# Kernel optimization log

Hardware: AMD Instinct MI355X
Metric: run time of the kernel (lower is better)

The kernel has to match this reference:

```python
import math
import jax, jax.numpy as jnp
import numpy as np

B, S, D, H = 4, 1024, 512, 8
DH = D // H  # 64
SQRT_DIM = math.sqrt(D)


def _relative_shift(pos_score):
    # pos_score: [B, H, S, S]
    b, h, s1, s2 = pos_score.shape
    zeros = jnp.zeros((b, h, s1, 1), dtype=pos_score.dtype)
    padded = jnp.concatenate([zeros, pos_score], axis=-1)      # [B,H,S,S+1]
    padded = padded.reshape(b, h, s2 + 1, s1)                  # [B,H,S+1,S]
    return padded[:, :, 1:].reshape(b, h, s1, s2)


def setup_inputs() -> dict:
    key = jax.random.key(0)
    ks = jax.random.split(key, 14)
    std = 0.02
    inp = {
        "query": jax.random.normal(ks[0], (B, S, D), jnp.float32),
        "key": jax.random.normal(ks[1], (B, S, D), jnp.float32),
        "value": jax.random.normal(ks[2], (B, S, D), jnp.float32),
        "pos_embedding": jax.random.normal(ks[3], (B, S, D), jnp.float32),
        # projection weights stored [in, out] so y = x @ W + b
        "Wq": jax.random.normal(ks[4], (D, D), jnp.float32) * std,
        "bq": jnp.zeros((D,), jnp.float32),
        "Wk": jax.random.normal(ks[5], (D, D), jnp.float32) * std,
        "bk": jnp.zeros((D,), jnp.float32),
        "Wv": jax.random.normal(ks[6], (D, D), jnp.float32) * std,
        "bv": jnp.zeros((D,), jnp.float32),
        "Wp": jax.random.normal(ks[7], (D, D), jnp.float32) * std,  # pos_proj, no bias
        "Wo": jax.random.normal(ks[8], (D, D), jnp.float32) * std,
        "bo": jnp.zeros((D,), jnp.float32),
        "u_bias": jax.random.normal(ks[9], (H, DH), jnp.float32) * std,
        "v_bias": jax.random.normal(ks[10], (H, DH), jnp.float32) * std,
    }
    return inp


def reference(query, key, value, pos_embedding, Wq, bq, Wk, bk, Wv, bv, Wp, Wo, bo, u_bias, v_bias):
    b = query.shape[0]
    q = (query @ Wq + bq).reshape(b, -1, H, DH)          # [B,S,H,DH]
    k = (key @ Wk + bk).reshape(b, -1, H, DH)            # [B,T,H,DH]
    v = (value @ Wv + bv).reshape(b, -1, H, DH)          # [B,T,H,DH]
    p = (pos_embedding @ Wp).reshape(b, -1, H, DH)       # [B,T,H,DH]

    # content score: (q + u) . k  -> [B,H,S,T]
    content_score = jnp.einsum('bshd,bthd->bhst', q + u_bias, k)
    # position score: (q + v) . pos -> [B,H,S,T], then relative shift
    pos_score = jnp.einsum('bshd,bthd->bhst', q + v_bias, p)
    pos_score = _relative_shift(pos_score)

    score = (content_score + pos_score) / SQRT_DIM
    attn = jax.nn.softmax(score, axis=-1)                # dropout p=0 (eval)

    context = jnp.einsum('bhst,bthd->bshd', attn, v).reshape(b, -1, D)
    out = context @ Wo + bo
    return (out, attn)
```

## Files before the change

kernel.cpp:

```cpp
#include <hip/hip_runtime.h>

#define B_  4
#define S_  1024
#define D_  512
#define H_  8
#define DH_ 64
#define SCALE 0.044194173824159216f

typedef short bf16x8 __attribute__((ext_vector_type(8)));
typedef float f32x4  __attribute__((ext_vector_type(4)));

__device__ __forceinline__ unsigned short f2bf(float x) {
    union { float f; unsigned int u; } v; v.f = x;
    unsigned int r = v.u + 0x7fffu + ((v.u >> 16) & 1u);
    return (unsigned short)(r >> 16);
}
__device__ __forceinline__ float bf2f(unsigned short h) {
    union { unsigned int u; float f; } v; v.u = ((unsigned int)h) << 16;
    return v.f;
}

__global__ __launch_bounds__(256) void convert_wt_k(
    const float* __restrict__ W0, const float* __restrict__ W1,
    const float* __restrict__ W2, const float* __restrict__ W3,
    const float* __restrict__ W4,
    unsigned short* __restrict__ T0, unsigned short* __restrict__ T1,
    unsigned short* __restrict__ T2, unsigned short* __restrict__ T3,
    unsigned short* __restrict__ T4)
{
    const float* W;
    unsigned short* T;
    switch (blockIdx.y) {
        case 0: W = W0; T = T0; break;
        case 1: W = W1; T = T1; break;
        case 2: W = W2; T = T2; break;
        case 3: W = W3; T = T3; break;
        default: W = W4; T = T4; break;
    }
    const int e = blockIdx.x * 256 + threadIdx.x;
    const int o = e >> 9, i = e & 511;
    T[(size_t)o * 512 + i] = f2bf(W[(size_t)i * 512 + o]);
}

__global__ __launch_bounds__(256) void proj_all_k(
    const float* __restrict__ Aq_, const float* __restrict__ Ak_,
    const float* __restrict__ Ap_, const float* __restrict__ Av_,
    const unsigned short* __restrict__ WqT, const unsigned short* __restrict__ WkT,
    const unsigned short* __restrict__ WpT, const unsigned short* __restrict__ WvT,
    const float* __restrict__ bq, const float* __restrict__ bk,
    const float* __restrict__ bv,
    const float* __restrict__ ub, const float* __restrict__ vb,
    unsigned short* __restrict__ qu, unsigned short* __restrict__ qv,
    unsigned short* __restrict__ kbf, unsigned short* __restrict__ pbf,
    unsigned short* __restrict__ vT)
{
    __shared__ unsigned short Ab[64][72];
    __shared__ unsigned short Bb[64][72];
    const int mode = blockIdx.z;
    const float* A;
    const unsigned short* BT;
    switch (mode) {
        case 0: A = Aq_; BT = WqT; break;
        case 1: A = Ak_; BT = WkT; break;
        case 2: A = Ap_; BT = WpT; break;
        default: A = Av_; BT = WvT; break;
    }
    const int tid = threadIdx.x;
    const int i0 = blockIdx.x * 64, j0 = blockIdx.y * 64;
    const int w = tid >> 6, lane = tid & 63, l15 = lane & 15, lhi = lane >> 4;
    const int mr0 = (w >> 1) * 32, nc0 = (w & 1) * 32;
    f32x4 acc[2][2] = {};

    for (int k0 = 0; k0 < 512; k0 += 64) {
        __syncthreads();
#pragma unroll
        for (int it = 0; it < 4; ++it) {
            const int s = tid + it * 256;
            const int row = s >> 4, f4 = (s & 15) * 4;
            float4 va = *(const float4*)&A[(size_t)(i0 + row) * 512 + k0 + f4];
            ushort4 hh;
            hh.x = f2bf(va.x); hh.y = f2bf(va.y); hh.z = f2bf(va.z); hh.w = f2bf(va.w);
            *(ushort4*)&Ab[row][f4] = hh;
        }
#pragma unroll
        for (int it = 0; it < 2; ++it) {
            const int s = tid + it * 256;
            const int row = s >> 3, g = (s & 7) * 8;
            *(bf16x8*)&Bb[row][g] = *(const bf16x8*)&BT[(size_t)(j0 + row) * 512 + k0 + g];
        }
        __syncthreads();
#pragma unroll
        for (int kk = 0; kk < 2; ++kk) {
            bf16x8 a0 = *(const bf16x8*)&Ab[mr0 + l15][kk * 32 + lhi * 8];
            bf16x8 a1 = *(const bf16x8*)&Ab[mr0 + 16 + l15][kk * 32 + lhi * 8];
            bf16x8 b0 = *(const bf16x8*)&Bb[nc0 + l15][kk * 32 + lhi * 8];
            bf16x8 b1 = *(const bf16x8*)&Bb[nc0 + 16 + l15][kk * 32 + lhi * 8];
            acc[0][0] = __builtin_amdgcn_mfma_f32_16x16x32_bf16(a0, b0, acc[0][0], 0, 0, 0);
            acc[0][1] = __builtin_amdgcn_mfma_f32_16x16x32_bf16(a0, b1, acc[0][1], 0, 0, 0);
            acc[1][0] = __builtin_amdgcn_mfma_f32_16x16x32_bf16(a1, b0, acc[1][0], 0, 0, 0);
            acc[1][1] = __builtin_amdgcn_mfma_f32_16x16x32_bf16(a1, b1, acc[1][1], 0, 0, 0);
        }
    }

#pragma unroll
    for (int m = 0; m < 2; ++m)
#pragma unroll
        for (int n = 0; n < 2; ++n)
#pragma unroll
            for (int r = 0; r < 4; ++r) {
                const int grow = i0 + mr0 + 16 * m + 4 * lhi + r;
                const int gcol = j0 + nc0 + 16 * n + l15;
                const int b = grow >> 10, s = grow & 1023;
                const int h = gcol >> 6, d = gcol & 63;
                const float v = acc[m][n][r];
                if (mode == 3) {
                    const size_t idx = (((size_t)(b * H_ + h)) * DH_ + d) * S_ + s;
                    vT[idx] = f2bf(v + bv[gcol]);
                } else {
                    const size_t idx = (((size_t)b * H_ + h) * S_ + s) * DH_ + d;
                    if (mode == 0) {
                        const float base = v + bq[gcol];
                        qu[idx] = f2bf(base + ub[gcol]);
                        qv[idx] = f2bf(base + vb[gcol]);
                    } else if (mode == 1) {
                        kbf[idx] = f2bf(v + bk[gcol]);
                    } else {
                        pbf[idx] = f2bf(v);
                    }
                }
            }
}

__global__ __launch_bounds__(256) void gemm_bf16_k(
    const unsigned short* __restrict__ A,
    const unsigned short* __restrict__ BT,
    const float* __restrict__ bias,
    float* __restrict__ C)
{
    __shared__ unsigned short Ab[64][72];
    __shared__ unsigned short Bb[64][72];
    const int tid = threadIdx.x;
    const int i0 = blockIdx.x * 64, j0 = blockIdx.y * 64;
    const int w = tid >> 6, lane = tid & 63, l15 = lane & 15, lhi = lane >> 4;
    const int mr0 = (w >> 1) * 32, nc0 = (w & 1) * 32;
    f32x4 acc[2][2] = {};

    for (int k0 = 0; k0 < 512; k0 += 64) {
        __syncthreads();
#pragma unroll
        for (int it = 0; it < 2; ++it) {
            const int s = tid + it * 256;
            const int row = s >> 3, g = (s & 7) * 8;
            *(bf16x8*)&Ab[row][g] = *(const bf16x8*)&A[(size_t)(i0 + row) * 512 + k0 + g];
            *(bf16x8*)&Bb[row][g] = *(const bf16x8*)&BT[(size_t)(j0 + row) * 512 + k0 + g];
        }
        __syncthreads();
#pragma unroll
        for (int kk = 0; kk < 2; ++kk) {
            bf16x8 a0 = *(const bf16x8*)&Ab[mr0 + l15][kk * 32 + lhi * 8];
            bf16x8 a1 = *(const bf16x8*)&Ab[mr0 + 16 + l15][kk * 32 + lhi * 8];
            bf16x8 b0 = *(const bf16x8*)&Bb[nc0 + l15][kk * 32 + lhi * 8];
            bf16x8 b1 = *(const bf16x8*)&Bb[nc0 + 16 + l15][kk * 32 + lhi * 8];
            acc[0][0] = __builtin_amdgcn_mfma_f32_16x16x32_bf16(a0, b0, acc[0][0], 0, 0, 0);
            acc[0][1] = __builtin_amdgcn_mfma_f32_16x16x32_bf16(a0, b1, acc[0][1], 0, 0, 0);
            acc[1][0] = __builtin_amdgcn_mfma_f32_16x16x32_bf16(a1, b0, acc[1][0], 0, 0, 0);
            acc[1][1] = __builtin_amdgcn_mfma_f32_16x16x32_bf16(a1, b1, acc[1][1], 0, 0, 0);
        }
    }

#pragma unroll
    for (int m = 0; m < 2; ++m)
#pragma unroll
        for (int n = 0; n < 2; ++n)
#pragma unroll
            for (int r = 0; r < 4; ++r) {
                const int grow = i0 + mr0 + 16 * m + 4 * lhi + r;
                const int gcol = j0 + nc0 + 16 * n + l15;
                C[(size_t)grow * 512 + gcol] = acc[m][n][r] + bias[gcol];
            }
}

#define RS 1032
#define QBLK 16

__global__ __launch_bounds__(512, 4) void score_fused_k(
    const unsigned short* __restrict__ qu_g,
    const unsigned short* __restrict__ qv_g,
    const unsigned short* __restrict__ kb_g,
    const unsigned short* __restrict__ pb_g,
    const unsigned short* __restrict__ vT_g,
    float* __restrict__ attn,
    unsigned short* __restrict__ ctx_g)
{
    __shared__ unsigned short Qu[16][72];
    __shared__ unsigned short Aq[32][72];
    __shared__ unsigned short Kb[128][72];
    __shared__ unsigned short Pb[128][72];
    __shared__ unsigned short Rfl[17 * RS];
    __shared__ float red[16][9];

    const int tid = threadIdx.x;
    const int i0 = blockIdx.x * QBLK;
    const int bh = blockIdx.y;
    const int w = tid >> 6, lane = tid & 63, l15 = lane & 15, lhi = lane >> 4;

    const unsigned short* qu_b = qu_g + (size_t)bh * S_ * DH_;
    const unsigned short* qv_b = qv_g + (size_t)bh * S_ * DH_;
    const unsigned short* kb_b = kb_g + (size_t)bh * S_ * DH_;
    const unsigned short* pb_b = pb_g + (size_t)bh * S_ * DH_;

    if (tid < 128) {
        const int r = tid >> 3, seg = (tid & 7) * 8;
        *(bf16x8*)&Qu[r][seg] = *(const bf16x8*)&qu_b[(size_t)(i0 + r) * DH_ + seg];
    }
    if (tid < 256) {
        const int r = tid >> 3, seg = (tid & 7) * 8;
        const int src = min(i0 + r, S_ - 1);
        *(bf16x8*)&Aq[r][seg] = *(const bf16x8*)&qv_b[(size_t)src * DH_ + seg];
    }

    bf16x8 kreg[2], preg[2];
#pragma unroll
    for (int it = 0; it < 2; ++it) {
        const int s = tid + it * 512;
        const int row = s >> 3, seg = (s & 7) * 8;
        kreg[it] = *(const bf16x8*)&kb_b[(size_t)row * DH_ + seg];
        preg[it] = *(const bf16x8*)&pb_b[(size_t)row * DH_ + seg];
    }

    f32x4 acc[8] = {};
    for (int jc = 0; jc < 8; ++jc) {
        __syncthreads();
#pragma unroll
        for (int it = 0; it < 2; ++it) {
            const int s = tid + it * 512;
            const int row = s >> 3, seg = (s & 7) * 8;
            *(bf16x8*)&Kb[row][seg] = kreg[it];
            *(bf16x8*)&Pb[row][seg] = preg[it];
        }
        if (jc < 7) {
#pragma unroll
            for (int it = 0; it < 2; ++it) {
                const int s = tid + it * 512;
                const int row = (jc + 1) * 128 + (s >> 3), seg = (s & 7) * 8;
                kreg[it] = *(const bf16x8*)&kb_b[(size_t)row * DH_ + seg];
                preg[it] = *(const bf16x8*)&pb_b[(size_t)row * DH_ + seg];
            }
        }
        __syncthreads();

        f32x4 racc[2] = {};
#pragma unroll
        for (int kk = 0; kk < 2; ++kk) {
            bf16x8 pfr = *(const bf16x8*)&Pb[16 * w + l15][kk * 32 + lhi * 8];
            bf16x8 kfr = *(const bf16x8*)&Kb[16 * w + l15][kk * 32 + lhi * 8];
            bf16x8 aq0 = *(const bf16x8*)&Aq[l15][kk * 32 + lhi * 8];
            bf16x8 aq1 = *(const bf16x8*)&Aq[16 + l15][kk * 32 + lhi * 8];
            bf16x8 qf  = *(const bf16x8*)&Qu[l15][kk * 32 + lhi * 8];
            racc[0] = __builtin_amdgcn_mfma_f32_16x16x32_bf16(aq0, pfr, racc[0], 0, 0, 0);
            racc[1] = __builtin_amdgcn_mfma_f32_16x16x32_bf16(aq1, pfr, racc[1], 0, 0, 0);
            acc[jc] = __builtin_amdgcn_mfma_f32_16x16x32_bf16(qf,  kfr, acc[jc], 0, 0, 0);
        }
#pragma unroll
        for (int m = 0; m < 2; ++m)
#pragma unroll
            for (int r = 0; r < 4; ++r) {
                const int row = 16 * m + 4 * lhi + r;
                if (row < 17)
                    Rfl[row * RS + jc * 128 + 16 * w + l15] = f2bf(racc[m][r]);
            }
    }
    __syncthreads();

    const int il = 4 * lhi;
    float rmax[4], rsum[4];
#pragma unroll
    for (int r = 0; r < 4; ++r) rmax[r] = -3.0e38f;

#pragma unroll
    for (int jc = 0; jc < 8; ++jc)
#pragma unroll
        for (int r = 0; r < 4; ++r) {
            const int row = il + r;
            const int i = i0 + row;
            const int j = jc * 128 + 16 * w + l15;
            float pos = 0.f;
            if (j <= i)          pos = bf2f(Rfl[row * RS + 1023 - i + j]);
            else if (j >= i + 2) pos = bf2f(Rfl[(row + 1) * RS + (j - i - 2)]);
            const float s = (acc[jc][r] + pos) * SCALE;
            acc[jc][r] = s;
            rmax[r] = fmaxf(rmax[r], s);
        }

#pragma unroll
    for (int r = 0; r < 4; ++r)
#pragma unroll
        for (int off = 1; off < 16; off <<= 1)
            rmax[r] = fmaxf(rmax[r], __shfl_xor(rmax[r], off));
    if (l15 == 0)
#pragma unroll
        for (int r = 0; r < 4; ++r) red[il + r][w] = rmax[r];
    __syncthreads();
#pragma unroll
    for (int r = 0; r < 4; ++r) {
        float mx = red[il + r][0];
#pragma unroll
        for (int ww = 1; ww < 8; ++ww) mx = fmaxf(mx, red[il + r][ww]);
        rmax[r] = mx;
        rsum[r] = 0.f;
    }
    __syncthreads();

#pragma unroll
    for (int jc = 0; jc < 8; ++jc)
#pragma unroll
        for (int r = 0; r < 4; ++r) {
            const float e = __expf(acc[jc][r] - rmax[r]);
            acc[jc][r] = e;
            rsum[r] += e;
        }
#pragma unroll
    for (int r = 0; r < 4; ++r)
#pragma unroll
        for (int off = 1; off < 16; off <<= 1)
            rsum[r] += __shfl_xor(rsum[r], off);
    if (l15 == 0)
#pragma unroll
        for (int r = 0; r < 4; ++r) red[il + r][w] = rsum[r];
    __syncthreads();

    float* attn_b = attn + (size_t)bh * S_ * S_;
#pragma unroll
    for (int r = 0; r < 4; ++r) {
        float sum = red[il + r][0];
#pragma unroll
        for (int ww = 1; ww < 8; ++ww) sum += red[il + r][ww];
        const float inv = 1.f / sum;
#pragma unroll
        for (int jc = 0; jc < 8; ++jc) {
            const int j = jc * 128 + 16 * w + l15;
            const float pn = acc[jc][r] * inv;
            attn_b[(size_t)(i0 + il + r) * S_ + j] = pn;
            Rfl[(il + r) * RS + j] = f2bf(pn);
        }
    }
    __syncthreads();

    const int b4 = bh >> 3, h4 = bh & 7;
    const int nblk = w & 3;
    const int kh = w >> 2;
    const unsigned short* vrow = vT_g + (size_t)bh * DH_ * S_
                               + (size_t)(16 * nblk + l15) * S_;
    f32x4 cacc = {};
#pragma unroll
    for (int ki = 0; ki < 16; ++ki) {
        const int t0 = kh * 512 + ki * 32 + lhi * 8;
        bf16x8 a  = *(const bf16x8*)&Rfl[l15 * RS + t0];
        bf16x8 bb = *(const bf16x8*)&vrow[t0];
        cacc = __builtin_amdgcn_mfma_f32_16x16x32_bf16(a, bb, cacc, 0, 0, 0);
    }
    float* fred = (float*)&Kb[0][0];
    if (kh == 0) {
#pragma unroll
        for (int r = 0; r < 4; ++r)
            fred[(nblk * 16 + 4 * lhi + r) * 16 + l15] = cacc[r];
    }
    __syncthreads();
    if (kh == 1) {
#pragma unroll
        for (int r = 0; r < 4; ++r) {
            const float vs = cacc[r] + fred[(nblk * 16 + 4 * lhi + r) * 16 + l15];
            const int srow = i0 + 4 * lhi + r;
            ctx_g[((size_t)(b4 * S_ + srow)) * D_ + h4 * DH_ + 16 * nblk + l15] = f2bf(vs);
        }
    }
}

extern "C" void kernel_launch(void* const* d_in, const int* in_sizes, int n_in,
                              void* d_out, int out_size, void* d_ws, size_t ws_size,
                              hipStream_t stream)
{
    const float* query = (const float*)d_in[0];
    const float* key_  = (const float*)d_in[1];
    const float* value = (const float*)d_in[2];
    const float* pose  = (const float*)d_in[3];
    const float* Wq = (const float*)d_in[4];
    const float* bq = (const float*)d_in[5];
    const float* Wk = (const float*)d_in[6];
    const float* bk = (const float*)d_in[7];
    const float* Wv = (const float*)d_in[8];
    const float* bv = (const float*)d_in[9];
    const float* Wp = (const float*)d_in[10];
    const float* Wo = (const float*)d_in[11];
    const float* bo = (const float*)d_in[12];
    const float* u_bias = (const float*)d_in[13];
    const float* v_bias = (const float*)d_in[14];

    const size_t NTOK = (size_t)B_ * S_ * D_;
    float* out  = (float*)d_out;
    float* attn = (float*)d_out + NTOK;

    unsigned short* qu  = (unsigned short*)d_ws;
    unsigned short* qv  = qu + NTOK;
    unsigned short* kbf = qv + NTOK;
    unsigned short* pbf = kbf + NTOK;
    unsigned short* WqT = pbf + NTOK;
    unsigned short* WkT = WqT + 262144;
    unsigned short* WpT = WkT + 262144;
    unsigned short* WvT = WpT + 262144;
    unsigned short* WoT = WvT + 262144;
    unsigned short* vT  = WoT + 262144;
    unsigned short* ctx = vT + NTOK;

    const dim3 blk256(256);
    const dim3 gproj(64, 8);

    convert_wt_k<<<dim3(1024, 5), blk256, 0, stream>>>(Wq, Wk, Wp, Wv, Wo,
                                                       WqT, WkT, WpT, WvT, WoT);

    proj_all_k<<<dim3(64, 8, 4), blk256, 0, stream>>>(
        query, key_, pose, value,
        WqT, WkT, WpT, WvT,
        bq, bk, bv, u_bias, v_bias,
        qu, qv, kbf, pbf, vT);

    score_fused_k<<<dim3(S_ / QBLK, B_ * H_), dim3(512), 0, stream>>>(
        qu, qv, kbf, pbf, vT, attn, ctx);

    gemm_bf16_k<<<gproj, blk256, 0, stream>>>(ctx, WoT, bo, out);
}
```

Before: 138.0 us.

## Tile weight transpose, block V layout, scatter shifted pos scores directly

```diff
diff --git a/kernel.cpp b/kernel.cpp
--- a/kernel.cpp
+++ b/kernel.cpp
@@ -28,18 +28,25 @@
     unsigned short* __restrict__ T2, unsigned short* __restrict__ T3,
     unsigned short* __restrict__ T4)
 {
+    __shared__ float tile[64][65];
     const float* W;
     unsigned short* T;
-    switch (blockIdx.y) {
+    switch (blockIdx.z) {
         case 0: W = W0; T = T0; break;
         case 1: W = W1; T = T1; break;
         case 2: W = W2; T = T2; break;
         case 3: W = W3; T = T3; break;
         default: W = W4; T = T4; break;
     }
-    const int e = blockIdx.x * 256 + threadIdx.x;
-    const int o = e >> 9, i = e & 511;
-    T[(size_t)o * 512 + i] = f2bf(W[(size_t)i * 512 + o]);
+    const int r0 = blockIdx.y * 64, c0 = blockIdx.x * 64;
+    const int tx = threadIdx.x & 63, ty = threadIdx.x >> 6;
+#pragma unroll
+    for (int it = 0; it < 16; ++it)
+        tile[ty + 4 * it][tx] = W[(size_t)(r0 + ty + 4 * it) * 512 + c0 + tx];
+    __syncthreads();
+#pragma unroll
+    for (int it = 0; it < 16; ++it)
+        T[(size_t)(c0 + ty + 4 * it) * 512 + r0 + tx] = f2bf(tile[tx][ty + 4 * it]);
 }
 
 __global__ __launch_bounds__(256) void proj_all_k(
@@ -52,7 +59,7 @@
     const float* __restrict__ ub, const float* __restrict__ vb,
     unsigned short* __restrict__ qu, unsigned short* __restrict__ qv,
     unsigned short* __restrict__ kbf, unsigned short* __restrict__ pbf,
-    unsigned short* __restrict__ vT)
+    unsigned short* __restrict__ v2)
 {
     __shared__ unsigned short Ab[64][72];
     __shared__ unsigned short Bb[64][72];
@@ -114,8 +121,8 @@
                 const int h = gcol >> 6, d = gcol & 63;
                 const float v = acc[m][n][r];
                 if (mode == 3) {
-                    const size_t idx = (((size_t)(b * H_ + h)) * DH_ + d) * S_ + s;
-                    vT[idx] = f2bf(v + bv[gcol]);
+                    const size_t idx = (((size_t)(b * H_ + h) * 32 + (s >> 5)) * 64 + d) * 32 + (s & 31);
+                    v2[idx] = f2bf(v + bv[gcol]);
                 } else {
                     const size_t idx = (((size_t)b * H_ + h) * S_ + s) * DH_ + d;
                     if (mode == 0) {
@@ -188,15 +195,13 @@
     const unsigned short* __restrict__ qv_g,
     const unsigned short* __restrict__ kb_g,
     const unsigned short* __restrict__ pb_g,
-    const unsigned short* __restrict__ vT_g,
+    const unsigned short* __restrict__ v2_g,
     float* __restrict__ attn,
     unsigned short* __restrict__ ctx_g)
 {
-    __shared__ unsigned short Qu[16][72];
-    __shared__ unsigned short Aq[32][72];
     __shared__ unsigned short Kb[128][72];
     __shared__ unsigned short Pb[128][72];
-    __shared__ unsigned short Rfl[17 * RS];
+    __shared__ unsigned short Rsh[16 * RS];
     __shared__ float red[16][9];
 
     const int tid = threadIdx.x;
@@ -209,14 +214,22 @@
     const unsigned short* kb_b = kb_g + (size_t)bh * S_ * DH_;
     const unsigned short* pb_b = pb_g + (size_t)bh * S_ * DH_;
 
-    if (tid < 128) {
-        const int r = tid >> 3, seg = (tid & 7) * 8;
-        *(bf16x8*)&Qu[r][seg] = *(const bf16x8*)&qu_b[(size_t)(i0 + r) * DH_ + seg];
-    }
-    if (tid < 256) {
-        const int r = tid >> 3, seg = (tid & 7) * 8;
-        const int src = min(i0 + r, S_ - 1);
-        *(bf16x8*)&Aq[r][seg] = *(const bf16x8*)&qv_b[(size_t)src * DH_ + seg];
+    if (tid < 16) {
+        const int j = i0 + tid + 1;
+        if (j <= 1023) Rsh[tid * RS + j] = 0;
+    }
+
+    bf16x8 qf[2], aq0[2], aq1[2];
+    {
+        const int qrow  = i0 + l15;
+        const int qrow1 = min(i0 + 16 + l15, S_ - 1);
+#pragma unroll
+        for (int kk = 0; kk < 2; ++kk) {
+            const int off = kk * 32 + lhi * 8;
+            qf[kk]  = *(const bf16x8*)&qu_b[(size_t)qrow  * DH_ + off];
+            aq0[kk] = *(const bf16x8*)&qv_b[(size_t)qrow  * DH_ + off];
+            aq1[kk] = *(const bf16x8*)&qv_b[(size_t)qrow1 * DH_ + off];
+        }
     }
 
     bf16x8 kreg[2], preg[2];
@@ -249,26 +262,30 @@
         }
         __syncthreads();
 
-        f32x4 racc[2] = {};
+        f32x4 racc0 = {}, racc1 = {};
 #pragma unroll
         for (int kk = 0; kk < 2; ++kk) {
             bf16x8 pfr = *(const bf16x8*)&Pb[16 * w + l15][kk * 32 + lhi * 8];
             bf16x8 kfr = *(const bf16x8*)&Kb[16 * w + l15][kk * 32 + lhi * 8];
-            bf16x8 aq0 = *(const bf16x8*)&Aq[l15][kk * 32 + lhi * 8];
-            bf16x8 aq1 = *(const bf16x8*)&Aq[16 + l15][kk * 32 + lhi * 8];
-            bf16x8 qf  = *(const bf16x8*)&Qu[l15][kk * 32 + lhi * 8];
-            racc[0] = __builtin_amdgcn_mfma_f32_16x16x32_bf16(aq0, pfr, racc[0], 0, 0, 0);
-            racc[1] = __builtin_amdgcn_mfma_f32_16x16x32_bf16(aq1, pfr, racc[1], 0, 0, 0);
-            acc[jc] = __builtin_amdgcn_mfma_f32_16x16x32_bf16(qf,  kfr, acc[jc], 0, 0, 0);
-        }
-#pragma unroll
-        for (int m = 0; m < 2; ++m)
-#pragma unroll
-            for (int r = 0; r < 4; ++r) {
-                const int row = 16 * m + 4 * lhi + r;
-                if (row < 17)
-                    Rfl[row * RS + jc * 128 + 16 * w + l15] = f2bf(racc[m][r]);
-            }
+            racc0 = __builtin_amdgcn_mfma_f32_16x16x32_bf16(aq0[kk], pfr, racc0, 0, 0, 0);
+            racc1 = __builtin_amdgcn_mfma_f32_16x16x32_bf16(aq1[kk], pfr, racc1, 0, 0, 0);
+            acc[jc] = __builtin_amdgcn_mfma_f32_16x16x32_bf16(qf[kk], kfr, acc[jc], 0, 0, 0);
+        }
+
+        const int u = jc * 128 + 16 * w + l15;
+#pragma unroll
+        for (int r = 0; r < 4; ++r) {
+            const int rl = 4 * lhi + r;
+            const int gr = i0 + rl;
+            const int jlo = u + gr - 1023;
+            const unsigned short val = f2bf(racc0[r]);
+            if (jlo >= 0)      Rsh[rl * RS + jlo] = val;
+            else if (rl >= 1)  Rsh[(rl - 1) * RS + (u + gr + 1)] = val;
+        }
+        if (lhi == 0) {
+            const int jhi = u + i0 + 17;
+            if (jhi <= 1023) Rsh[15 * RS + jhi] = f2bf(racc1[0]);
+        }
     }
     __syncthreads();
 
@@ -282,11 +299,8 @@
 #pragma unroll
         for (int r = 0; r < 4; ++r) {
             const int row = il + r;
-            const int i = i0 + row;
             const int j = jc * 128 + 16 * w + l15;
-            float pos = 0.f;
-            if (j <= i)          pos = bf2f(Rfl[row * RS + 1023 - i + j]);
-            else if (j >= i + 2) pos = bf2f(Rfl[(row + 1) * RS + (j - i - 2)]);
+            const float pos = bf2f(Rsh[row * RS + j]);
             const float s = (acc[jc][r] + pos) * SCALE;
             acc[jc][r] = s;
             rmax[r] = fmaxf(rmax[r], s);
@@ -341,7 +355,7 @@
             const int j = jc * 128 + 16 * w + l15;
             const float pn = acc[jc][r] * inv;
             attn_b[(size_t)(i0 + il + r) * S_ + j] = pn;
-            Rfl[(il + r) * RS + j] = f2bf(pn);
+            Rsh[(il + r) * RS + j] = f2bf(pn);
         }
     }
     __syncthreads();
@@ -349,15 +363,23 @@
     const int b4 = bh >> 3, h4 = bh & 7;
     const int nblk = w & 3;
     const int kh = w >> 2;
-    const unsigned short* vrow = vT_g + (size_t)bh * DH_ * S_
-                               + (size_t)(16 * nblk + l15) * S_;
+    const unsigned short* v2b = v2_g + (size_t)bh * 32 * 2048;
+    const int dd = 16 * nblk + l15;
     f32x4 cacc = {};
 #pragma unroll
-    for (int ki = 0; ki < 16; ++ki) {
-        const int t0 = kh * 512 + ki * 32 + lhi * 8;
-        bf16x8 a  = *(const bf16x8*)&Rfl[l15 * RS + t0];
-        bf16x8 bb = *(const bf16x8*)&vrow[t0];
-        cacc = __builtin_amdgcn_mfma_f32_16x16x32_bf16(a, bb, cacc, 0, 0, 0);
+    for (int half = 0; half < 2; ++half) {
+        bf16x8 bbuf[8];
+#pragma unroll
+        for (int ki = 0; ki < 8; ++ki) {
+            const int tb = kh * 16 + half * 8 + ki;
+            bbuf[ki] = *(const bf16x8*)&v2b[(size_t)tb * 2048 + dd * 32 + lhi * 8];
+        }
+#pragma unroll
+        for (int ki = 0; ki < 8; ++ki) {
+            const int t0 = (kh * 16 + half * 8 + ki) * 32 + lhi * 8;
+            bf16x8 a = *(const bf16x8*)&Rsh[l15 * RS + t0];
+            cacc = __builtin_amdgcn_mfma_f32_16x16x32_bf16(a, bbuf[ki], cacc, 0, 0, 0);
+        }
     }
     float* fred = (float*)&Kb[0][0];
     if (kh == 0) {
@@ -409,23 +431,23 @@
     unsigned short* WpT = WkT + 262144;
     unsigned short* WvT = WpT + 262144;
     unsigned short* WoT = WvT + 262144;
-    unsigned short* vT  = WoT + 262144;
-    unsigned short* ctx = vT + NTOK;
+    unsigned short* v2  = WoT + 262144;
+    unsigned short* ctx = v2 + NTOK;
 
     const dim3 blk256(256);
     const dim3 gproj(64, 8);
 
-    convert_wt_k<<<dim3(1024, 5), blk256, 0, stream>>>(Wq, Wk, Wp, Wv, Wo,
+    convert_wt_k<<<dim3(8, 8, 5), blk256, 0, stream>>>(Wq, Wk, Wp, Wv, Wo,
                                                        WqT, WkT, WpT, WvT, WoT);
 
     proj_all_k<<<dim3(64, 8, 4), blk256, 0, stream>>>(
         query, key_, pose, value,
         WqT, WkT, WpT, WvT,
         bq, bk, bv, u_bias, v_bias,
-        qu, qv, kbf, pbf, vT);
+        qu, qv, kbf, pbf, v2);
 
     score_fused_k<<<dim3(S_ / QBLK, B_ * H_), dim3(512), 0, stream>>>(
-        qu, qv, kbf, pbf, vT, attn, ctx);
+        qu, qv, kbf, pbf, v2, attn, ctx);
 
     gemm_bf16_k<<<gproj, blk256, 0, stream>>>(ctx, WoT, bo, out);
 }
```

Result: faster. 131.8 us (-4.5%).
